# Performance work log

Measured on AMD Instinct MI355X. Metric: run time of the kernel, lower is better.

The kernel has to match this reference:

```python
import jax, jax.numpy as jnp
import numpy as np

N = 50000
F_IN = 512
H1, C1 = 8, 16          # layer-1 heads / per-head channels
H2, C2 = 1, 40          # layer-2 heads / num_classes
NEG_SLOPE = 0.2


def setup_inputs() -> dict:
    key = jax.random.key(0)
    ks = jax.random.split(key, 10)
    E = 800000
    x = jax.random.normal(ks[0], (N, F_IN), dtype=jnp.float32)
    edge_index = jax.random.randint(ks[1], (2, E), 0, N, dtype=jnp.int64)
    s1 = 1.0 / np.sqrt(F_IN)
    s2 = 1.0 / np.sqrt(H1 * C1)
    return {
        "x": x,
        "edge_index": edge_index,
        "W1": jax.random.normal(ks[2], (F_IN, H1 * C1), dtype=jnp.float32) * s1,
        "att_src1": jax.random.normal(ks[3], (H1, C1), dtype=jnp.float32) * s2,
        "att_dst1": jax.random.normal(ks[4], (H1, C1), dtype=jnp.float32) * s2,
        "b1": jnp.zeros((H1 * C1,), dtype=jnp.float32),
        "W2": jax.random.normal(ks[5], (H1 * C1, H2 * C2), dtype=jnp.float32) * s2,
        "att_src2": jax.random.normal(ks[6], (H2, C2), dtype=jnp.float32) * (1.0 / np.sqrt(C2)),
        "att_dst2": jax.random.normal(ks[7], (H2, C2), dtype=jnp.float32) * (1.0 / np.sqrt(C2)),
        "b2": jnp.zeros((H2 * C2,), dtype=jnp.float32),
    }


def _gat_conv(x, W, att_src, att_dst, b, src, dst, H, C):
    # x: [N, Fin] -> h: [N, H, C]
    h = (x @ W).reshape(N, H, C)
    a_src = jnp.einsum("nhc,hc->nh", h, att_src)  # [N, H]
    a_dst = jnp.einsum("nhc,hc->nh", h, att_dst)
    e = a_src[src] + a_dst[dst]                    # [E, H]
    e = jax.nn.leaky_relu(e, NEG_SLOPE)
    # segment softmax over edges sharing the same target node (dst)
    m = jax.ops.segment_max(e, dst, num_segments=N)         # [N, H]
    ex = jnp.exp(e - m[dst])
    denom = jax.ops.segment_sum(ex, dst, num_segments=N)    # [N, H]
    alpha = ex / (denom[dst] + 1e-16)                        # [E, H]
    msg = h[src] * alpha[..., None]                          # [E, H, C]
    out = jax.ops.segment_sum(msg, dst, num_segments=N)     # [N, H, C]
    return out.reshape(N, H * C) + b


def reference(x, edge_index, W1, att_src1, att_dst1, b1, W2, att_src2, att_dst2, b2):
    # add self-loops (PyG GATConv default)
    loop = jnp.arange(N, dtype=edge_index.dtype)
    src = jnp.concatenate([edge_index[0], loop])
    dst = jnp.concatenate([edge_index[1], loop])
    h = _gat_conv(x, W1, att_src1, att_dst1, b1, src, dst, H1, C1)
    h = jax.nn.elu(h)
    h = _gat_conv(h, W2, att_src2, att_dst2, b2, src, dst, H2, C2)
    return jax.nn.log_softmax(h, axis=1)
```

## Files before the change

kernel.cpp:

```cpp
#include <hip/hip_runtime.h>
#include <math.h>

#define N_NODES 50000
#define FIN 512
#define NE 800000
#define ETOT 850000
#define F1 128
#define H1 8
#define F2 40
#define BCAP 64
#define NBIN 391
#define BINCAP 3072

typedef __attribute__((ext_vector_type(8))) short bf16x8;
typedef __attribute__((ext_vector_type(4))) float f32x4;

__device__ inline ushort f2bf(float f){
  union{float f; unsigned u;} v; v.f=f;
  return (ushort)((v.u + 0x8000u) >> 16);
}
__device__ inline float bflo(uint u){ union{uint a;float f;} v; v.a = u << 16;         return v.f; }
__device__ inline float bfhi(uint u){ union{uint a;float f;} v; v.a = u & 0xffff0000u; return v.f; }
__device__ inline float bf1(ushort u){ union{uint a;float f;} v; v.a = ((uint)u) << 16; return v.f; }

__device__ inline bf16x8 cvt8(float4 a, float4 b){
  union{ushort u[8]; bf16x8 v;} r;
  r.u[0]=f2bf(a.x); r.u[1]=f2bf(a.y); r.u[2]=f2bf(a.z); r.u[3]=f2bf(a.w);
  r.u[4]=f2bf(b.x); r.u[5]=f2bf(b.y); r.u[6]=f2bf(b.z); r.u[7]=f2bf(b.w);
  return r.v;
}


__global__ __launch_bounds__(1024) void k_pro(const int* __restrict__ src, const int* __restrict__ dst,
                                              int* __restrict__ binCursor, uint* __restrict__ binbuf,
                                              const float* __restrict__ W1, const float* __restrict__ W2,
                                              ushort* __restrict__ Wtb, ushort* __restrict__ Wt2){
  __shared__ int hist[512];
  __shared__ int base[512];
  int bx = blockIdx.x, t = threadIdx.x;

  if(bx < 104){
    if(t < 512) hist[t] = 0;
    __syncthreads();

    uint pk[8]; int bn[8];
    int i0 = bx*8192 + t;
    #pragma unroll
    for(int k=0;k<8;k++){
      int i = i0 + k*1024;
      int d = -1, s = 0;
      if(i < NE){ d = dst[i]; s = src[i]; }
      else if(i < ETOT){ d = i - NE; s = d; }
      if(d >= 0){
        bn[k] = d >> 7;
        pk[k] = ((uint)d << 16) | (uint)s;
        atomicAdd(&hist[bn[k]], 1);
      } else bn[k] = -1;
    }
    __syncthreads();
    if(t < 512){
      int h = hist[t];
      base[t] = (t < NBIN && h > 0) ? atomicAdd(&binCursor[t], h) : 0;
    }
    __syncthreads();
    if(t < 512) hist[t] = 0;
    __syncthreads();
    #pragma unroll
    for(int k=0;k<8;k++){
      if(bn[k] >= 0){
        int off = atomicAdd(&hist[bn[k]], 1);
        binbuf[(size_t)bn[k]*BINCAP + base[bn[k]] + off] = pk[k];
      }
    }
  } else {
    int id = (bx - 104)*1024 + t;
    if(id < 65536){
      int k = id >> 7, n = id & 127;
      Wtb[(size_t)(k>>3)*1024 + n*8 + (k&7)] = f2bf(W1[id]);
    } else {
      int id2 = id - 65536;
      if(id2 < 6144){
        int j = id2 & 7;
        int tt = id2 >> 3;
        int n = tt % 48;
        int t2 = tt / 48;
        int quad = t2 & 3, ks = t2 >> 2;
        int k = ks*32 + quad*8 + j;
        Wt2[id2] = (n < F2) ? f2bf(W2[k*F2 + n]) : (ushort)0;
      }
    }
  }
}


__global__ __launch_bounds__(256) void k_g1b(const int* __restrict__ binCursor, const uint* __restrict__ binbuf,
                                             int* __restrict__ cnt, ushort* __restrict__ bucket,
                                             const float* __restrict__ x, const ushort* __restrict__ Wtb,
                                             const float* __restrict__ as_w, const float* __restrict__ ad_w,
                                             ushort* __restrict__ h1b,
                                             float* __restrict__ a_src, float* __restrict__ a_dst){
  __shared__ __align__(16) char smem[17408];
  int bxg = blockIdx.x;

  if(bxg < NBIN){
    int* lcnt  = (int*)smem;
    ushort* lb = (ushort*)(smem + 512);
    int b = bxg, t = threadIdx.x;
    if(t < 128) lcnt[t] = 0;
    __syncthreads();
    int m = min(binCursor[b], BINCAP);
    const uint* p = binbuf + (size_t)b*BINCAP;
    for(int i=t; i<m; i+=256){
      uint pk = p[i];
      int dl = (pk >> 16) & 127;
      int pos = atomicAdd(&lcnt[dl], 1);
      if(pos < BCAP) lb[dl*66 + pos] = (ushort)(pk & 0xFFFF);
    }
    __syncthreads();
    int n0 = b << 7;
    int nrows = min(128, N_NODES - n0);
    if(t < nrows) cnt[n0 + t] = lcnt[t];
    const uint* s4 = (const uint*)(smem + 512);
    uint* d4 = (uint*)(bucket + ((size_t)n0 << 6));
    int total = nrows * 32;
    for(int i=t; i<total; i+=256){
      int r = i >> 5, c = i & 31;
      d4[i] = s4[r*33 + c];
    }
    return;
  }

  float* AsmF = (float*)smem;
  int tid = threadIdx.x;
  int bx  = bxg - NBIN;
  int wave = tid >> 6, lane = tid & 63;
  int l15 = lane & 15, quad = lane >> 4;

  f32x4 acc[2][2];
  #pragma unroll
  for(int i=0;i<2;i++)
    #pragma unroll
    for(int j=0;j<2;j++) acc[i][j] = (f32x4){0.f,0.f,0.f,0.f};

  int srow = tid >> 4;
  int scl  = (tid & 15) << 2;
  int ssc  = scl ^ ((srow & 3) << 2);
  int sg0  = min(bx*32 + srow,      N_NODES-1);
  int sg1  = min(bx*32 + 16 + srow, N_NODES-1);
  const float* gp0 = x + (size_t)sg0*FIN + ssc;
  const float* gp1 = x + (size_t)sg1*FIN + ssc;
  char* lbase = smem + (wave << 10);

#define STAGE_A(buf, kt) do{                                                            \
    __builtin_amdgcn_global_load_lds((const __attribute__((address_space(1))) void*)(gp0 + (kt)), \
        (__attribute__((address_space(3))) void*)(lbase + (buf)*8192), 16, 0, 0);       \
    __builtin_amdgcn_global_load_lds((const __attribute__((address_space(1))) void*)(gp1 + (kt)), \
        (__attribute__((address_space(3))) void*)(lbase + (buf)*8192 + 4096), 16, 0, 0);\
  }while(0)

  const ushort* wpB = Wtb + (size_t)quad*1024 + (size_t)(wave*32 + l15)*8;

  STAGE_A(0, 0);
  bf16x8 bcur[2][2];
  #pragma unroll
  for(int ks=0;ks<2;ks++)
    #pragma unroll
    for(int tn=0;tn<2;tn++)
      bcur[ks][tn] = *(const bf16x8*)(wpB + ks*4096 + tn*128);
  __syncthreads();

  for(int kt=0; kt<FIN; kt+=64){
    int cur = (kt >> 6) & 1;
    bool hn = (kt + 64) < FIN;

    if(hn) STAGE_A(cur^1, kt+64);

    bf16x8 bnext[2][2];
    if(hn){
      #pragma unroll
      for(int ks=0;ks<2;ks++)
        #pragma unroll
        for(int tn=0;tn<2;tn++)
          bnext[ks][tn] = *(const bf16x8*)(wpB + (size_t)(kt+64)*128 + ks*4096 + tn*128);
    }

    bf16x8 af[2][2];
    #pragma unroll
    for(int tm=0;tm<2;tm++)
      #pragma unroll
      for(int ks=0;ks<2;ks++){
        int r  = tm*16 + l15;
        int cA = (ks*32 + quad*8) ^ ((r & 3) << 2);
        const float* fp = AsmF + cur*2048 + r*64;
        float4 fa = *(const float4*)(fp + cA);
        float4 fb = *(const float4*)(fp + (cA ^ 4));
        af[tm][ks] = cvt8(fa, fb);
      }

    #pragma unroll
    for(int ks=0;ks<2;ks++)
      #pragma unroll
      for(int tm=0;tm<2;tm++)
        #pragma unroll
        for(int tn=0;tn<2;tn++)
          acc[tm][tn] = __builtin_amdgcn_mfma_f32_16x16x32_bf16(af[tm][ks], bcur[ks][tn], acc[tm][tn], 0,0,0);

    __syncthreads();
    #pragma unroll
    for(int ks=0;ks<2;ks++)
      #pragma unroll
      for(int tn=0;tn<2;tn++)
        bcur[ks][tn] = bnext[ks][tn];
  }

  float wsv[2], wdv[2];
  #pragma unroll
  for(int tn=0;tn<2;tn++){
    int h = wave*2 + tn;
    wsv[tn] = as_w[h*16 + l15];
    wdv[tn] = ad_w[h*16 + l15];
  }

  #pragma unroll
  for(int tm=0;tm<2;tm++){
    #pragma unroll
    for(int r=0;r<4;r++){
      int row = bx*32 + tm*16 + quad*4 + r;
      bool ok = row < N_NODES;
      #pragma unroll
      for(int tn=0;tn<2;tn++){
        float v = acc[tm][tn][r];
        if(ok){
          int col = wave*32 + tn*16 + l15;
          h1b[(size_t)row*F1 + col] = f2bf(v);
        }
        float ss = v * wsv[tn];
        float dd = v * wdv[tn];
        #pragma unroll
        for(int m=8;m;m>>=1){ ss += __shfl_xor(ss, m); dd += __shfl_xor(dd, m); }
        if(ok && l15 == 0){
          int h = wave*2 + tn;
          a_src[(size_t)row*H1 + h] = ss;
          a_dst[(size_t)row*H1 + h] = dd;
        }
      }
    }
  }
#undef STAGE_A
}


__global__ __launch_bounds__(256) void k_agg1(const ushort* __restrict__ h1b, const float* __restrict__ a_src,
                                              const float* __restrict__ a_dst,
                                              const int* __restrict__ cnt, const ushort* __restrict__ bucket,
                                              const float* __restrict__ b1, ushort* __restrict__ gb){
  int wave = threadIdx.x >> 6, lane = threadIdx.x & 63;
  int n = blockIdx.x*4 + wave;
  if(n >= N_NODES) return;
  int hl = lane >> 3;
  float adv = a_dst[n*H1 + hl];
  int deg = min(cnt[n], BCAP);
  int sv = (int)bucket[(n << 6) + lane];
  const uint* h1u = (const uint*)h1b;

  float ws0=0.f, ax0=0.f, ay0=0.f;
  float ws1=0.f, ax1=0.f, ay1=0.f;
  float ws2=0.f, ax2=0.f, ay2=0.f;
  float ws3=0.f, ax3=0.f, ay3=0.f;
  int j = 0;
  for(; j+3<deg; j+=4){
    int s0 = __shfl(sv, j),   s1 = __shfl(sv, j+1);
    int s2 = __shfl(sv, j+2), s3 = __shfl(sv, j+3);
    float e0 = a_src[s0*H1 + hl] + adv;
    float e1 = a_src[s1*H1 + hl] + adv;
    float e2 = a_src[s2*H1 + hl] + adv;
    float e3 = a_src[s3*H1 + hl] + adv;
    e0 = e0 > 0.f ? e0 : 0.2f*e0;  e1 = e1 > 0.f ? e1 : 0.2f*e1;
    e2 = e2 > 0.f ? e2 : 0.2f*e2;  e3 = e3 > 0.f ? e3 : 0.2f*e3;
    float w0=__expf(e0), w1=__expf(e1), w2=__expf(e2), w3=__expf(e3);
    uint u0 = h1u[(size_t)s0*64 + lane];
    uint u1 = h1u[(size_t)s1*64 + lane];
    uint u2 = h1u[(size_t)s2*64 + lane];
    uint u3 = h1u[(size_t)s3*64 + lane];
    ax0 += w0*bflo(u0); ay0 += w0*bfhi(u0); ws0 += w0;
    ax1 += w1*bflo(u1); ay1 += w1*bfhi(u1); ws1 += w1;
    ax2 += w2*bflo(u2); ay2 += w2*bfhi(u2); ws2 += w2;
    ax3 += w3*bflo(u3); ay3 += w3*bfhi(u3); ws3 += w3;
  }
  for(; j<deg; j++){
    int s0 = __shfl(sv, j);
    float e0 = a_src[s0*H1 + hl] + adv;
    e0 = e0 > 0.f ? e0 : 0.2f*e0;
    float w0 = __expf(e0);
    uint u0 = h1u[(size_t)s0*64 + lane];
    ax0 += w0*bflo(u0); ay0 += w0*bfhi(u0); ws0 += w0;
  }
  float wsum = (ws0+ws1)+(ws2+ws3);
  float inv = 1.f/(wsum + 1e-16f);
  int c0 = lane*2;
  float o0 = ((ax0+ax1)+(ax2+ax3))*inv + b1[c0];
  float o1 = ((ay0+ay1)+(ay2+ay3))*inv + b1[c0+1];
  o0 = o0 > 0.f ? o0 : expm1f(o0);
  o1 = o1 > 0.f ? o1 : expm1f(o1);
  uint up = (uint)f2bf(o0) | ((uint)f2bf(o1) << 16);
  ((uint*)gb)[(size_t)n*64 + lane] = up;
}


__global__ __launch_bounds__(256) void k_gemm2(const ushort* __restrict__ gb, const ushort* __restrict__ Wt2,
                                               const float* __restrict__ as_w, const float* __restrict__ ad_w,
                                               ushort* __restrict__ h2b,
                                               float* __restrict__ a_src, float* __restrict__ a_dst){
  int tid = threadIdx.x;
  int wave = tid >> 6, lane = tid & 63;
  int l15 = lane & 15, quad = lane >> 4;
  int row0 = blockIdx.x*64 + wave*16;
  int arow = min(row0 + l15, N_NODES-1);
  const ushort* ap = gb + (size_t)arow*F1 + quad*8;

  f32x4 acc[3];
  #pragma unroll
  for(int tn=0;tn<3;tn++) acc[tn] = (f32x4){0.f,0.f,0.f,0.f};

  #pragma unroll
  for(int ks=0;ks<4;ks++){
    bf16x8 af = *(const bf16x8*)(ap + ks*32);
    #pragma unroll
    for(int tn=0;tn<3;tn++){
      bf16x8 bf = *(const bf16x8*)(Wt2 + ((size_t)(ks*4+quad)*48 + tn*16 + l15)*8);
      acc[tn] = __builtin_amdgcn_mfma_f32_16x16x32_bf16(af, bf, acc[tn], 0,0,0);
    }
  }

  float ws2v[3], wd2v[3];
  #pragma unroll
  for(int tn=0;tn<3;tn++){
    int col = tn*16 + l15;
    ws2v[tn] = (col < F2) ? as_w[col] : 0.f;
    wd2v[tn] = (col < F2) ? ad_w[col] : 0.f;
  }

  #pragma unroll
  for(int r=0;r<4;r++){
    int row = row0 + quad*4 + r;
    bool ok = row < N_NODES;
    float ss = 0.f, dd = 0.f;
    #pragma unroll
    for(int tn=0;tn<3;tn++){
      float v = acc[tn][r];
      int col = tn*16 + l15;
      if(ok && col < F2) h2b[(size_t)row*F2 + col] = f2bf(v);
      ss += v * ws2v[tn];
      dd += v * wd2v[tn];
    }
    #pragma unroll
    for(int m=8;m;m>>=1){ ss += __shfl_xor(ss, m); dd += __shfl_xor(dd, m); }
    if(ok && l15 == 0){
      a_src[row] = ss;
      a_dst[row] = dd;
    }
  }
}


__global__ __launch_bounds__(256) void k_agg2(const ushort* __restrict__ h2b, const float* __restrict__ a_src,
                                              const float* __restrict__ a_dst,
                                              const int* __restrict__ cnt, const ushort* __restrict__ bucket,
                                              const float* __restrict__ b2, float* __restrict__ out){
  int wave = threadIdx.x >> 6, lane = threadIdx.x & 63;
  int n = blockIdx.x*4 + wave;
  if(n >= N_NODES) return;
  float adv = a_dst[n];
  int deg = min(cnt[n], BCAP);
  int sv = (int)bucket[(n << 6) + lane];
  int c = (lane < F2) ? lane : (F2-1);

  float ws0=0.f, ac0=0.f, ws1=0.f, ac1=0.f, ws2=0.f, ac2=0.f, ws3=0.f, ac3=0.f;
  int j = 0;
  for(; j+3<deg; j+=4){
    int s0 = __shfl(sv, j),   s1 = __shfl(sv, j+1);
    int s2 = __shfl(sv, j+2), s3 = __shfl(sv, j+3);
    float e0 = a_src[s0] + adv, e1 = a_src[s1] + adv;
    float e2 = a_src[s2] + adv, e3 = a_src[s3] + adv;
    e0 = e0 > 0.f ? e0 : 0.2f*e0;  e1 = e1 > 0.f ? e1 : 0.2f*e1;
    e2 = e2 > 0.f ? e2 : 0.2f*e2;  e3 = e3 > 0.f ? e3 : 0.2f*e3;
    float w0=__expf(e0), w1=__expf(e1), w2=__expf(e2), w3=__expf(e3);
    ac0 += w0*bf1(h2b[(size_t)s0*F2 + c]); ws0 += w0;
    ac1 += w1*bf1(h2b[(size_t)s1*F2 + c]); ws1 += w1;
    ac2 += w2*bf1(h2b[(size_t)s2*F2 + c]); ws2 += w2;
    ac3 += w3*bf1(h2b[(size_t)s3*F2 + c]); ws3 += w3;
  }
  for(; j<deg; j++){
    int s0 = __shfl(sv, j);
    float e0 = a_src[s0] + adv;
    e0 = e0 > 0.f ? e0 : 0.2f*e0;
    float w0 = __expf(e0);
    ac0 += w0*bf1(h2b[(size_t)s0*F2 + c]); ws0 += w0;
  }
  float v = ((ac0+ac1)+(ac2+ac3))/(((ws0+ws1)+(ws2+ws3)) + 1e-16f) + b2[c];
  float mv = (lane < F2) ? v : -INFINITY;
  #pragma unroll
  for(int off=32; off; off>>=1) mv = fmaxf(mv, __shfl_xor(mv, off));
  float ex = (lane < F2) ? __expf(v - mv) : 0.f;
  #pragma unroll
  for(int off=32; off; off>>=1) ex += __shfl_xor(ex, off);
  if(lane < F2) out[(size_t)n*F2 + lane] = v - mv - logf(ex);
}


extern "C" void kernel_launch(void* const* d_in, const int* in_sizes, int n_in,
                              void* d_out, int out_size, void* d_ws, size_t ws_size,
                              hipStream_t stream) {
  const float* x        = (const float*)d_in[0];
  const int*   eidx     = (const int*)d_in[1];
  const float* W1       = (const float*)d_in[2];
  const float* att_src1 = (const float*)d_in[3];
  const float* att_dst1 = (const float*)d_in[4];
  const float* b1       = (const float*)d_in[5];
  const float* W2       = (const float*)d_in[6];
  const float* att_src2 = (const float*)d_in[7];
  const float* att_dst2 = (const float*)d_in[8];
  const float* b2       = (const float*)d_in[9];
  float* out = (float*)d_out;

  const int* src = eidx;
  const int* dst = eidx + NE;

  ushort* h1b  = (ushort*)d_ws;
  ushort* h2b  = h1b + 6400000;
  ushort* gb   = h2b + 2000000;
  ushort* Wtb  = gb + 6400000;
  ushort* bucket = Wtb + 65536;
  float* a_src1 = (float*)(bucket + 3200000);
  float* a_dst1 = a_src1 + 400000;
  float* a_src2 = a_dst1 + 400000;
  float* a_dst2 = a_src2 + 50000;
  int* cnt      = (int*)(a_dst2 + 50000);
  int* binCursor= cnt + 50002;
  uint* binbuf  = (uint*)(binCursor + 512);
  ushort* Wt2   = (ushort*)(binbuf + (size_t)NBIN*BINCAP);

  hipMemsetAsync(binCursor, 0, 512*sizeof(int), stream);

  k_pro<<<174, 1024, 0, stream>>>(src, dst, binCursor, binbuf, W1, W2, Wtb, Wt2);

  k_g1b<<<NBIN + 1563, 256, 0, stream>>>(binCursor, binbuf, cnt, bucket,
                                         x, Wtb, att_src1, att_dst1, h1b, a_src1, a_dst1);

  k_agg1<<<(N_NODES+3)/4, 256, 0, stream>>>(h1b, a_src1, a_dst1, cnt, bucket, b1, gb);

  k_gemm2<<<(N_NODES+63)/64, 256, 0, stream>>>(gb, Wt2, att_src2, att_dst2, h2b, a_src2, a_dst2);
  k_agg2 <<<(N_NODES+3)/4, 256, 0, stream>>>(h2b, a_src2, a_dst2, cnt, bucket, b2, out);
}
```

Before: 282.0 us.

## Triple-buffer x tile staging in layer-1 GEMM with explicit vmcnt barriers

Moves the layer-1 projection GEMM from double to triple buffering of the x tile in LDS. Loads are issued two k-steps ahead, and the full __syncthreads is replaced by a partial s_waitcnt vmcnt plus s_barrier, so the next-next tile's global-to-LDS loads can stay in flight. The goal is to hide global load latency behind the MFMA work. In exchange the shared block grows to 24 KB, which may lower occupancy for both the GEMM and the binning blocks in this fused kernel. It also relies on hand-counted vmcnt values.

```diff
diff --git a/kernel.cpp b/kernel.cpp
--- a/kernel.cpp
+++ b/kernel.cpp
@@ -99,7 +99,7 @@
                                              const float* __restrict__ as_w, const float* __restrict__ ad_w,
                                              ushort* __restrict__ h1b,
                                              float* __restrict__ a_src, float* __restrict__ a_dst){
-  __shared__ __align__(16) char smem[17408];
+  __shared__ __align__(16) char smem[24576];
   int bxg = blockIdx.x;
 
   if(bxg < NBIN){
@@ -151,29 +151,38 @@
   const float* gp1 = x + (size_t)sg1*FIN + ssc;
   char* lbase = smem + (wave << 10);
 
-#define STAGE_A(buf, kt) do{                                                            \
+#define STAGE_A(p, kt) do{                                                              \
     __builtin_amdgcn_global_load_lds((const __attribute__((address_space(1))) void*)(gp0 + (kt)), \
-        (__attribute__((address_space(3))) void*)(lbase + (buf)*8192), 16, 0, 0);       \
+        (__attribute__((address_space(3))) void*)(lbase + (p)*8192), 16, 0, 0);         \
     __builtin_amdgcn_global_load_lds((const __attribute__((address_space(1))) void*)(gp1 + (kt)), \
-        (__attribute__((address_space(3))) void*)(lbase + (buf)*8192 + 4096), 16, 0, 0);\
+        (__attribute__((address_space(3))) void*)(lbase + (p)*8192 + 4096), 16, 0, 0);  \
   }while(0)
 
   const ushort* wpB = Wtb + (size_t)quad*1024 + (size_t)(wave*32 + l15)*8;
 
   STAGE_A(0, 0);
+  STAGE_A(1, 64);
   bf16x8 bcur[2][2];
   #pragma unroll
   for(int ks=0;ks<2;ks++)
     #pragma unroll
     for(int tn=0;tn<2;tn++)
       bcur[ks][tn] = *(const bf16x8*)(wpB + ks*4096 + tn*128);
-  __syncthreads();
-
+  __builtin_amdgcn_sched_barrier(0);
+  asm volatile("s_waitcnt vmcnt(0)" ::: "memory");
+  __builtin_amdgcn_s_barrier();
+  __builtin_amdgcn_sched_barrier(0);
+
+  int cur = 0;
+  #pragma unroll 1
   for(int kt=0; kt<FIN; kt+=64){
-    int cur = (kt >> 6) & 1;
-    bool hn = (kt + 64) < FIN;
-
-    if(hn) STAGE_A(cur^1, kt+64);
+    bool hn = (kt + 64)  < FIN;
+    bool h2 = (kt + 128) < FIN;
+
+    if(h2){
+      int nb = cur + 2; if(nb >= 3) nb -= 3;
+      STAGE_A(nb, kt+128);
+    }
 
     bf16x8 bnext[2][2];
     if(hn){
@@ -205,12 +214,19 @@
         for(int tn=0;tn<2;tn++)
           acc[tm][tn] = __builtin_amdgcn_mfma_f32_16x16x32_bf16(af[tm][ks], bcur[ks][tn], acc[tm][tn], 0,0,0);
 
-    __syncthreads();
-    #pragma unroll
-    for(int ks=0;ks<2;ks++)
+    if(hn){
+      __builtin_amdgcn_sched_barrier(0);
+      if(h2) asm volatile("s_waitcnt vmcnt(6)" ::: "memory");
+      else   asm volatile("s_waitcnt vmcnt(4)" ::: "memory");
+      __builtin_amdgcn_s_barrier();
+      __builtin_amdgcn_sched_barrier(0);
       #pragma unroll
-      for(int tn=0;tn<2;tn++)
-        bcur[ks][tn] = bnext[ks][tn];
+      for(int ks=0;ks<2;ks++)
+        #pragma unroll
+        for(int tn=0;tn<2;tn++)
+          bcur[ks][tn] = bnext[ks][tn];
+    }
+    cur = cur + 1; if(cur >= 3) cur -= 3;
   }
 
   float wsv[2], wdv[2];
```

Result: no change. 284.0 us (+0.7%).
